# Performance work log

Measured on AMD Instinct MI355X. Metric: run time of the kernel, lower is better.

## Reference

```python
import jax, jax.numpy as jnp
import numpy as np

B, L, D = 2, 2048, 1024
DI, N, DCONV, DTR, I = 2048, 16, 4, 64, 4096  # d_inner, d_state, d_conv, dt_rank, ffn intermediate
EPS = 1e-5


def _ln(x, w, b):
    m = jnp.mean(x, axis=-1, keepdims=True)
    v = jnp.var(x, axis=-1, keepdims=True)
    return (x - m) * jax.lax.rsqrt(v + EPS) * w + b


def _mamba_dir(h, inproj_w, outproj_w, conv_w, conv_b, xproj_w, dtproj_w, dtproj_b, A_log, Dp):
    # h: (B,L,D). Standard Mamba (S6) forward for one direction.
    xz = jnp.einsum('bld,ed->ble', h, inproj_w)          # (B,L,2*DI)
    x, z = jnp.split(xz, 2, axis=-1)                     # each (B,L,DI)
    # causal depthwise conv1d, kernel size DCONV
    xp = jnp.pad(x, ((0, 0), (DCONV - 1, 0), (0, 0)))
    x = sum(xp[:, k:k + L, :] * conv_w[:, k] for k in range(DCONV)) + conv_b
    x = jax.nn.silu(x)
    x_dbl = jnp.einsum('bld,ed->ble', x, xproj_w)        # (B,L,DTR+2N)
    dt, Bm, Cm = jnp.split(x_dbl, [DTR, DTR + N], axis=-1)
    dt = jax.nn.softplus(jnp.einsum('blr,dr->bld', dt, dtproj_w) + dtproj_b)  # (B,L,DI)
    A = -jnp.exp(A_log)                                  # (DI,N)

    def step(s, inp):
        xt, dtt, bt, ct = inp                            # (B,DI),(B,DI),(B,N),(B,N)
        dA = jnp.exp(dtt[..., None] * A)                 # (B,DI,N)
        s = s * dA + (dtt * xt)[..., None] * bt[:, None, :]
        y = jnp.einsum('bdn,bn->bd', s, ct)
        return s, y

    xs = (x.transpose(1, 0, 2), dt.transpose(1, 0, 2), Bm.transpose(1, 0, 2), Cm.transpose(1, 0, 2))
    s0 = jnp.zeros((x.shape[0], DI, N), dtype=x.dtype)
    _, ys = jax.lax.scan(step, s0, xs)                   # ys: (L,B,DI)
    y = ys.transpose(1, 0, 2) + x * Dp
    y = y * jax.nn.silu(z)
    return jnp.einsum('bld,ed->ble', y, outproj_w)       # (B,L,D)


def _forward(hidden_states, residual, inproj_w, outproj_w,
             conv_w_f, conv_b_f, xproj_w_f, dtproj_w_f, dtproj_b_f, A_log_f, D_f,
             conv_w_r, conv_b_r, xproj_w_r, dtproj_w_r, dtproj_b_r, A_log_r, D_r,
             ln1_w, ln1_b, ln2_w, ln2_b, gate_w, up_w, down_w):
    # inner mamba_ssm Block: add -> LN -> mixer
    res1 = hidden_states + residual
    h = _ln(res1, ln1_w, ln1_b)
    out_f = _mamba_dir(h, inproj_w, outproj_w, conv_w_f, conv_b_f, xproj_w_f,
                       dtproj_w_f, dtproj_b_f, A_log_f, D_f)
    out_r = _mamba_dir(h[:, ::-1, :], inproj_w, outproj_w, conv_w_r, conv_b_r, xproj_w_r,
                       dtproj_w_r, dtproj_b_r, A_log_r, D_r)[:, ::-1, :]
    h = out_f + out_r                                    # bidirectional 'add'
    # outer MambaBlock: add -> LN -> MLP
    residual2 = h + res1
    h = _ln(residual2, ln2_w, ln2_b)
    gate = jax.nn.silu(jnp.einsum('bld,id->bli', h, gate_w))
    up = jnp.einsum('bld,id->bli', h, up_w)
    h = jnp.einsum('bli,di->bld', gate * up, down_w)
    return h, residual2


def setup_inputs() -> dict:
    key = jax.random.key(0)
    ks = jax.random.split(key, 24)

    def nrm(k, shape, scale=0.02):
        return jax.random.normal(k, shape, dtype=jnp.float32) * scale

    inp = {
        'hidden_states': jax.random.normal(ks[0], (B, L, D), jnp.float32),
        'residual': jax.random.normal(ks[1], (B, L, D), jnp.float32),
        'inproj_w': nrm(ks[2], (2 * DI, D)),
        'outproj_w': nrm(ks[3], (D, DI)),
    }
    for i, sfx in enumerate(('f', 'r')):
        o = 4 + i * 7
        inp[f'conv_w_{sfx}'] = nrm(ks[o], (DI, DCONV), 0.2)
        inp[f'conv_b_{sfx}'] = nrm(ks[o + 1], (DI,), 0.02)
        inp[f'xproj_w_{sfx}'] = nrm(ks[o + 2], (DTR + 2 * N, DI))
        inp[f'dtproj_w_{sfx}'] = nrm(ks[o + 3], (DI, DTR), 0.1)
        inp[f'dtproj_b_{sfx}'] = jnp.full((DI,), -4.0, jnp.float32) + nrm(ks[o + 4], (DI,), 0.1)
        inp[f'A_log_{sfx}'] = jnp.log(jnp.tile(jnp.arange(1, N + 1, dtype=jnp.float32)[None, :], (DI, 1)))
        inp[f'D_{sfx}'] = jnp.ones((DI,), jnp.float32)
    inp['ln1_w'] = jnp.ones((D,), jnp.float32)
    inp['ln1_b'] = jnp.zeros((D,), jnp.float32)
    inp['ln2_w'] = jnp.ones((D,), jnp.float32)
    inp['ln2_b'] = jnp.zeros((D,), jnp.float32)
    inp['gate_w'] = nrm(ks[18], (I, D))
    inp['up_w'] = nrm(ks[19], (I, D))
    inp['down_w'] = nrm(ks[20], (D, I))
    return inp


def reference(hidden_states, residual, inproj_w, outproj_w,
              conv_w_f, conv_b_f, xproj_w_f, dtproj_w_f, dtproj_b_f, A_log_f, D_f,
              conv_w_r, conv_b_r, xproj_w_r, dtproj_w_r, dtproj_b_r, A_log_r, D_r,
              ln1_w, ln1_b, ln2_w, ln2_b, gate_w, up_w, down_w):
    return _forward(hidden_states, residual, inproj_w, outproj_w,
                    conv_w_f, conv_b_f, xproj_w_f, dtproj_w_f, dtproj_b_f, A_log_f, D_f,
                    conv_w_r, conv_b_r, xproj_w_r, dtproj_w_r, dtproj_b_r, A_log_r, D_r,
                    ln1_w, ln1_b, ln2_w, ln2_b, gate_w, up_w, down_w)
```

## Files before the change

kernel.cpp:

```cpp
#include <hip/hip_runtime.h>
#include <hip/hip_bf16.h>

#define BB 2
#define LL 2048
#define DD 1024
#define DI_ 2048
#define NS 16
#define DTR_ 64
#define XDW 96
#define BLR 4096
#define NC 64
#define CLEN 32

typedef __attribute__((ext_vector_type(8))) short s16x8;
typedef __attribute__((ext_vector_type(4))) float f32x4;

#define L2E 1.44269504f
#define LN2 0.69314718f

__device__ __forceinline__ float bfraw2f(unsigned short u){
  union { unsigned int i; float f; } x; x.i = ((unsigned int)u) << 16; return x.f;
}
__device__ __forceinline__ unsigned short f2bfraw(float f){
  union { float f; unsigned int i; } x; x.f = f;
  unsigned int u = x.i;
  u += 0x7FFFu + ((u >> 16) & 1u);
  return (unsigned short)(u >> 16);
}
__device__ __forceinline__ float exp2_(float x){ return __builtin_amdgcn_exp2f(x); }
__device__ __forceinline__ float silu_(float a){
  float e = exp2_(-a * L2E);
  return a * __builtin_amdgcn_rcpf(1.f + e);
}
__device__ __forceinline__ float softplus_(float v){
  if (v > 20.f) return v;
  float e = exp2_(v * L2E);
  return LN2 * __builtin_amdgcn_logf(1.f + e);
}

typedef __attribute__((address_space(1))) void gas_void;
typedef __attribute__((address_space(3))) void las_void;
__device__ __forceinline__ void gl_lds16(const unsigned short* g, unsigned short* l){
  __builtin_amdgcn_global_load_lds((gas_void*)g, (las_void*)l, 16, 0, 0);
}

struct CvtArgs {
  const float* s[9];
  unsigned short* d;
  unsigned int off[10];
};
__global__ __launch_bounds__(256) void k_wcvt(CvtArgs a, unsigned int total4){
  unsigned int g = blockIdx.x*256 + threadIdx.x;
  if (g >= total4) return;
  unsigned int e = g*4;
  int sgi = 0;
  #pragma unroll
  for (int i=1;i<9;i++) if (e >= a.off[i]) sgi = i;
  const float* s = a.s[sgi];
  f32x4 v = *(const f32x4*)(s + (e - a.off[sgi]));
  unsigned long long o = 0;
  #pragma unroll
  for (int k=0;k<4;k++) o |= ((unsigned long long)f2bfraw(v[k])) << (16*k);
  *(unsigned long long*)(a.d + e) = o;
}

__global__ __launch_bounds__(256) void k_add_ln(
  const float* __restrict__ pa, const float* __restrict__ pb,
  const float* __restrict__ w, const float* __restrict__ bi,
  float* __restrict__ res_f,
  unsigned short* __restrict__ h_out)
{
  int row = blockIdx.x, tid = threadIdx.x;
  int lane = tid & 63, wave = tid >> 6;
  int c0 = tid * 4;
  size_t base = (size_t)row * DD + c0;
  float v[4];
  f32x4 av = *(const f32x4*)(pa + base);
  f32x4 bv = *(const f32x4*)(pb + base);
  #pragma unroll
  for (int k=0;k<4;k++) v[k] = av[k] + bv[k];
  float s_ = v[0]+v[1]+v[2]+v[3];
  #pragma unroll
  for (int off=32; off>0; off>>=1) s_ += __shfl_down(s_, off, 64);
  __shared__ float red1[4], red2[4];
  if (lane==0) red1[wave] = s_;
  __syncthreads();
  float mean = (red1[0]+red1[1]+red1[2]+red1[3]) * (1.f/DD);
  float ss = 0.f;
  #pragma unroll
  for (int k=0;k<4;k++){ float dv = v[k]-mean; ss += dv*dv; }
  #pragma unroll
  for (int off=32; off>0; off>>=1) ss += __shfl_down(ss, off, 64);
  if (lane==0) red2[wave] = ss;
  __syncthreads();
  float var = (red2[0]+red2[1]+red2[2]+red2[3]) * (1.f/DD);
  float rs = rsqrtf(var + 1e-5f);
  f32x4 wv = *(const f32x4*)(w + c0);
  f32x4 biv = *(const f32x4*)(bi + c0);
  unsigned long long hv = 0;
  #pragma unroll
  for (int k=0;k<4;k++){
    float hn = (v[k]-mean)*rs*wv[k] + biv[k];
    hv |= ((unsigned long long)(unsigned short)f2bfraw(hn)) << (16*k);
  }
  *(unsigned long long*)(h_out + base) = hv;
  if (res_f){ f32x4 o = {v[0],v[1],v[2],v[3]}; *(f32x4*)(res_f + base) = o; }
}

__global__ __launch_bounds__(256) void k_add_ln4(
  const float* __restrict__ pa, const float* __restrict__ pb,
  const float* __restrict__ w, const float* __restrict__ bi,
  float* __restrict__ res_f,
  unsigned short* __restrict__ h_out)
{
  int row = blockIdx.x, tid = threadIdx.x;
  int lane = tid & 63, wave = tid >> 6;
  int c0 = tid * 4;
  size_t base = (size_t)row * DD + c0;
  const size_t MN = 4194304;
  f32x4 p0 = *(const f32x4*)(pa + base);
  f32x4 p1 = *(const f32x4*)(pa + MN + base);
  f32x4 p2 = *(const f32x4*)(pa + 2*MN + base);
  f32x4 p3 = *(const f32x4*)(pa + 3*MN + base);
  f32x4 bv = *(const f32x4*)(pb + base);
  float v[4];
  #pragma unroll
  for (int k=0;k<4;k++) v[k] = ((p0[k]+p1[k]) + (p2[k]+p3[k])) + bv[k];
  float s_ = v[0]+v[1]+v[2]+v[3];
  #pragma unroll
  for (int off=32; off>0; off>>=1) s_ += __shfl_down(s_, off, 64);
  __shared__ float red1[4], red2[4];
  if (lane==0) red1[wave] = s_;
  __syncthreads();
  float mean = (red1[0]+red1[1]+red1[2]+red1[3]) * (1.f/DD);
  float ss = 0.f;
  #pragma unroll
  for (int k=0;k<4;k++){ float dv = v[k]-mean; ss += dv*dv; }
  #pragma unroll
  for (int off=32; off>0; off>>=1) ss += __shfl_down(ss, off, 64);
  if (lane==0) red2[wave] = ss;
  __syncthreads();
  float var = (red2[0]+red2[1]+red2[2]+red2[3]) * (1.f/DD);
  float rs = rsqrtf(var + 1e-5f);
  f32x4 wv = *(const f32x4*)(w + c0);
  f32x4 biv = *(const f32x4*)(bi + c0);
  unsigned long long hv = 0;
  #pragma unroll
  for (int k=0;k<4;k++){
    float hn = (v[k]-mean)*rs*wv[k] + biv[k];
    hv |= ((unsigned long long)(unsigned short)f2bfraw(hn)) << (16*k);
  }
  *(unsigned long long*)(h_out + base) = hv;
  if (res_f){ f32x4 o = {v[0],v[1],v[2],v[3]}; *(f32x4*)(res_f + base) = o; }
}

__global__ __launch_bounds__(256) void k_red4(
  const float* __restrict__ p, float* __restrict__ o)
{
  size_t e = ((size_t)blockIdx.x*256 + threadIdx.x)*4;
  const size_t MN = 4194304;
  f32x4 a = *(const f32x4*)(p + e);
  f32x4 b = *(const f32x4*)(p + MN + e);
  f32x4 c = *(const f32x4*)(p + 2*MN + e);
  f32x4 d = *(const f32x4*)(p + 3*MN + e);
  f32x4 r;
  #pragma unroll
  for (int k=0;k<4;k++) r[k] = (a[k]+b[k]) + (c[k]+d[k]);
  *(f32x4*)(o + e) = r;
}

template<int EPI>
__global__ __launch_bounds__(256) void k_gemm_lds(
  const unsigned short* __restrict__ A0, const unsigned short* __restrict__ A1,
  const unsigned short* __restrict__ W0, const unsigned short* __restrict__ W1,
  float* __restrict__ Cf0, float* __restrict__ Cf1,
  unsigned short* __restrict__ Cb0, unsigned short* __restrict__ Cb1,
  const float* __restrict__ bias0, const float* __restrict__ bias1,
  int M, int N, int K, int lda)
{
  __shared__ unsigned short S[17408];
  const unsigned short* A = blockIdx.z ? A1 : A0;
  const unsigned short* W = blockIdx.z ? W1 : W0;
  float* Cf = blockIdx.z ? Cf1 : Cf0;
  unsigned short* Cb = blockIdx.z ? Cb1 : Cb0;
  const float* bias = blockIdx.z ? bias1 : bias0;

  int tid = threadIdx.x;
  int wave = tid >> 6, lane = tid & 63;
  int l16 = lane & 15, quad = lane >> 4;
  int wm = (wave >> 1) * 64, wn = (wave & 1) * 64;
  int m0 = blockIdx.y * 128, n0 = blockIdx.x * 128;

  int colsw = (((lane & 7) ^ (lane >> 3)) * 8);
  const unsigned short* ag[4];
  const unsigned short* wg[4];
  unsigned short* al[4];
  unsigned short* bl[4];
  #pragma unroll
  for (int c = 0; c < 4; c++){
    int ca = wave*4 + c;
    int ra = m0 + ca*8 + (lane>>3); if (ra >= M) ra = M-1;
    int rb = n0 + ca*8 + (lane>>3); if (rb >= N) rb = N-1;
    ag[c] = A + (size_t)ra*lda + colsw;
    wg[c] = W + (size_t)rb*K + colsw;
    al[c] = S + ca*512;
    bl[c] = S + 8192 + ca*512;
  }

  int swz = (l16 & 7) * 8;
  f32x4 acc[4][4] = {};

  for (int k0 = 0; k0 < K; k0 += 64){
    #pragma unroll
    for (int c = 0; c < 4; c++){
      gl_lds16(ag[c] + k0, al[c]);
      gl_lds16(wg[c] + k0, bl[c]);
    }
    __syncthreads();
    #pragma unroll
    for (int s = 0; s < 2; s++){
      int koff = (s*32 + quad*8) ^ swz;
      s16x8 af[4], bw[4];
      #pragma unroll
      for (int i = 0; i < 4; i++)
        af[i] = *(const s16x8*)(S + (wm + i*16 + l16)*64 + koff);
      #pragma unroll
      for (int j = 0; j < 4; j++)
        bw[j] = *(const s16x8*)(S + 8192 + (wn + j*16 + l16)*64 + koff);
      #pragma unroll
      for (int i = 0; i < 4; i++)
        #pragma unroll
        for (int j = 0; j < 4; j++)
          acc[i][j] = __builtin_amdgcn_mfma_f32_16x16x32_bf16(af[i], bw[j], acc[i][j], 0, 0, 0);
    }
    __syncthreads();
  }

  if (Cb){
    #pragma unroll
    for (int j=0;j<4;j++){
      int colL = wn + j*16 + l16;
      float bval = (EPI==1) ? bias[n0 + colL] : 0.f;
      #pragma unroll
      for (int i=0;i<4;i++){
        #pragma unroll
        for (int r=0;r<4;r++){
          int rowL = wm + i*16 + quad*4 + r;
          float v = acc[i][j][r];
          if (EPI==1) v = softplus_(v + bval);
          S[rowL*136 + colL] = f2bfraw(v);
        }
      }
    }
    __syncthreads();
    #pragma unroll
    for (int p=0;p<8;p++){
      int e = p*2048 + tid*8;
      int rowL = e >> 7, colL = e & 127;
      s16x8 val = *(const s16x8*)(S + rowL*136 + colL);
      *(s16x8*)(Cb + (size_t)(m0 + rowL)*N + n0 + colL) = val;
    }
  } else {
    #pragma unroll
    for (int j=0;j<4;j++){
      int col = n0 + wn + j*16 + l16;
      if (col >= N) continue;
      float bval = (EPI==1) ? bias[col] : 0.f;
      #pragma unroll
      for (int i=0;i<4;i++){
        #pragma unroll
        for (int r=0;r<4;r++){
          int rowi = m0 + wm + i*16 + quad*4 + r;
          float v = acc[i][j][r];
          if (EPI==1) v = softplus_(v + bval);
          Cf[(size_t)rowi*N + col] = v;
        }
      }
    }
  }
}

__global__ __launch_bounds__(256) void k_gemm_sk2(
  const unsigned short* __restrict__ A, const unsigned short* __restrict__ W,
  float* __restrict__ P,
  int M, int N, int K, int lda, int kwin)
{
  __shared__ unsigned short S[16384];
  int tid = threadIdx.x;
  int wave = tid >> 6, lane = tid & 63;
  int l16 = lane & 15, quad = lane >> 4;
  int wm = (wave >> 1) * 64, wn = (wave & 1) * 64;

  int bid = blockIdx.x;
  int xcd = bid & 7;
  int idx = bid >> 3;
  int nt  = idx & 7;
  int ks  = (idx >> 3) & 3;
  int mg  = idx >> 5;
  int m0 = (xcd*4 + mg) * 128;
  int n0 = nt * 128;
  int kbase = ks * kwin;
  float* Cf = P + (size_t)ks * ((size_t)M * N);

  int colsw = (((lane & 7) ^ (lane >> 3)) * 8);
  const unsigned short* ag[4];
  const unsigned short* wg[4];
  unsigned short* al[4];
  unsigned short* bl[4];
  #pragma unroll
  for (int c = 0; c < 4; c++){
    int ca = wave*4 + c;
    int ra = m0 + ca*8 + (lane>>3);
    int rb = n0 + ca*8 + (lane>>3);
    ag[c] = A + (size_t)ra*lda + kbase + colsw;
    wg[c] = W + (size_t)rb*K + kbase + colsw;
    al[c] = S + ca*512;
    bl[c] = S + 8192 + ca*512;
  }

  int swz = (l16 & 7) * 8;
  f32x4 acc[4][4] = {};

  for (int k0 = 0; k0 < kwin; k0 += 64){
    #pragma unroll
    for (int c = 0; c < 4; c++){
      gl_lds16(ag[c] + k0, al[c]);
      gl_lds16(wg[c] + k0, bl[c]);
    }
    __syncthreads();
    #pragma unroll
    for (int s = 0; s < 2; s++){
      int koff = (s*32 + quad*8) ^ swz;
      s16x8 af[4], bw[4];
      #pragma unroll
      for (int i = 0; i < 4; i++)
        af[i] = *(const s16x8*)(S + (wm + i*16 + l16)*64 + koff);
      #pragma unroll
      for (int j = 0; j < 4; j++)
        bw[j] = *(const s16x8*)(S + 8192 + (wn + j*16 + l16)*64 + koff);
      #pragma unroll
      for (int i = 0; i < 4; i++)
        #pragma unroll
        for (int j = 0; j < 4; j++)
          acc[i][j] = __builtin_amdgcn_mfma_f32_16x16x32_bf16(af[i], bw[j], acc[i][j], 0, 0, 0);
    }
    __syncthreads();
  }

  #pragma unroll
  for (int j=0;j<4;j++){
    int col = n0 + wn + j*16 + l16;
    #pragma unroll
    for (int i=0;i<4;i++){
      #pragma unroll
      for (int r=0;r<4;r++){
        int rowi = m0 + wm + i*16 + quad*4 + r;
        Cf[(size_t)rowi*N + col] = acc[i][j][r];
      }
    }
  }
}

__global__ __launch_bounds__(512) void k_gemm_gateup(
  const unsigned short* __restrict__ A, const unsigned short* __restrict__ Wg,
  const unsigned short* __restrict__ Wu, unsigned short* __restrict__ Cb,
  int M, int N, int K, int lda)
{
  __shared__ unsigned short S[24576];
  int tid = threadIdx.x;
  int wave = tid >> 6, lane = tid & 63;
  int l16 = lane & 15, quad = lane >> 4;
  int w4 = wave & 3;
  int isUp = wave >> 2;
  int wm = (w4 >> 1) * 64, wn = (w4 & 1) * 64;
  int m0 = blockIdx.y * 128, n0 = blockIdx.x * 128;

  int colsw = (((lane & 7) ^ (lane >> 3)) * 8);
  const unsigned short* ag[2];
  const unsigned short* gg[2];
  const unsigned short* ug[2];
  unsigned short* al[2];
  unsigned short* glp[2];
  unsigned short* ulp[2];
  #pragma unroll
  for (int c = 0; c < 2; c++){
    int ca = wave*2 + c;
    int ra = m0 + ca*8 + (lane>>3);
    int rb = n0 + ca*8 + (lane>>3);
    ag[c] = A + (size_t)ra*lda + colsw;
    gg[c] = Wg + (size_t)rb*K + colsw;
    ug[c] = Wu + (size_t)rb*K + colsw;
    al[c]  = S + ca*512;
    glp[c] = S + 8192 + ca*512;
    ulp[c] = S + 16384 + ca*512;
  }

  int swz = (l16 & 7) * 8;
  int bbase = isUp ? 16384 : 8192;
  f32x4 acc[4][4] = {};

  for (int k0 = 0; k0 < K; k0 += 64){
    #pragma unroll
    for (int c = 0; c < 2; c++){
      gl_lds16(ag[c] + k0, al[c]);
      gl_lds16(gg[c] + k0, glp[c]);
      gl_lds16(ug[c] + k0, ulp[c]);
    }
    __syncthreads();
    #pragma unroll
    for (int s = 0; s < 2; s++){
      int koff = (s*32 + quad*8) ^ swz;
      s16x8 af[4], bw[4];
      #pragma unroll
      for (int i = 0; i < 4; i++)
        af[i] = *(const s16x8*)(S + (wm + i*16 + l16)*64 + koff);
      #pragma unroll
      for (int j = 0; j < 4; j++)
        bw[j] = *(const s16x8*)(S + bbase + (wn + j*16 + l16)*64 + koff);
      #pragma unroll
      for (int i = 0; i < 4; i++)
        #pragma unroll
        for (int j = 0; j < 4; j++)
          acc[i][j] = __builtin_amdgcn_mfma_f32_16x16x32_bf16(af[i], bw[j], acc[i][j], 0, 0, 0);
    }
    __syncthreads();
  }

  if (isUp){
    #pragma unroll
    for (int j=0;j<4;j++){
      int colL = wn + j*16 + l16;
      #pragma unroll
      for (int i=0;i<4;i++){
        #pragma unroll
        for (int r=0;r<4;r++){
          int rowL = wm + i*16 + quad*4 + r;
          S[rowL*136 + colL] = f2bfraw(acc[i][j][r]);
        }
      }
    }
  }
  __syncthreads();
  if (!isUp){
    #pragma unroll
    for (int j=0;j<4;j++){
      int colL = wn + j*16 + l16;
      #pragma unroll
      for (int i=0;i<4;i++){
        #pragma unroll
        for (int r=0;r<4;r++){
          int rowL = wm + i*16 + quad*4 + r;
          int idx = rowL*136 + colL;
          float u = bfraw2f(S[idx]);
          S[idx] = f2bfraw(silu_(acc[i][j][r]) * u);
        }
      }
    }
  }
  __syncthreads();
  #pragma unroll
  for (int p=0;p<4;p++){
    int e = p*4096 + tid*8;
    int rowL = e >> 7, colL = e & 127;
    s16x8 val = *(const s16x8*)(S + rowL*136 + colL);
    *(s16x8*)(Cb + (size_t)(m0 + rowL)*N + n0 + colL) = val;
  }
}

__global__ __launch_bounds__(256) void k_gemm_splitk(
  const unsigned short* __restrict__ A0, const unsigned short* __restrict__ A1,
  const unsigned short* __restrict__ W0, const unsigned short* __restrict__ W1,
  float* __restrict__ C0, float* __restrict__ C1,
  int M, int N, int K, int lda, int kwin)
{
  __shared__ unsigned short S[16384];
  const unsigned short* A = blockIdx.z ? A1 : A0;
  const unsigned short* W = blockIdx.z ? W1 : W0;
  float* C = blockIdx.z ? C1 : C0;

  int tid = threadIdx.x;
  int wave = tid >> 6, lane = tid & 63;
  int l16 = lane & 15, quad = lane >> 4;
  int wm = (wave >> 1) * 64, wn = (wave & 1) * 64;
  int m0 = blockIdx.y * 128;
  int kbase = blockIdx.x * kwin;

  int colsw = (((lane & 7) ^ (lane >> 3)) * 8);
  const unsigned short* ag[4];
  const unsigned short* wg[4];
  unsigned short* al[4];
  unsigned short* bl[4];
  #pragma unroll
  for (int c = 0; c < 4; c++){
    int ca = wave*4 + c;
    int ra = m0 + ca*8 + (lane>>3);
    int rb = ca*8 + (lane>>3); if (rb >= N) rb = N-1;
    ag[c] = A + (size_t)ra*lda + kbase + colsw;
    wg[c] = W + (size_t)rb*K + kbase + colsw;
    al[c] = S + ca*512;
    bl[c] = S + 8192 + ca*512;
  }

  int swz = (l16 & 7) * 8;
  f32x4 acc[4][4] = {};

  for (int k0 = 0; k0 < kwin; k0 += 64){
    #pragma unroll
    for (int c = 0; c < 4; c++){
      gl_lds16(ag[c] + k0, al[c]);
      gl_lds16(wg[c] + k0, bl[c]);
    }
    __syncthreads();
    #pragma unroll
    for (int s = 0; s < 2; s++){
      int koff = (s*32 + quad*8) ^ swz;
      s16x8 af[4], bw[4];
      #pragma unroll
      for (int i = 0; i < 4; i++)
        af[i] = *(const s16x8*)(S + (wm + i*16 + l16)*64 + koff);
      #pragma unroll
      for (int j = 0; j < 4; j++)
        bw[j] = *(const s16x8*)(S + 8192 + (wn + j*16 + l16)*64 + koff);
      #pragma unroll
      for (int i = 0; i < 4; i++)
        #pragma unroll
        for (int j = 0; j < 4; j++)
          acc[i][j] = __builtin_amdgcn_mfma_f32_16x16x32_bf16(af[i], bw[j], acc[i][j], 0, 0, 0);
    }
    __syncthreads();
  }

  #pragma unroll
  for (int j=0;j<4;j++){
    int col = wn + j*16 + l16;
    if (col >= N) continue;
    #pragma unroll
    for (int i=0;i<4;i++){
      #pragma unroll
      for (int r=0;r<4;r++){
        int rowi = m0 + wm + i*16 + quad*4 + r;
        atomicAdd(&C[(size_t)rowi*N + col], acc[i][j][r]);
      }
    }
  }
}

__global__ __launch_bounds__(256) void k_xdcvt(
  const float* __restrict__ xd, unsigned short* __restrict__ xdb)
{
  unsigned int e = (blockIdx.x*256 + threadIdx.x)*4;
  f32x4 v = *(const f32x4*)(xd + e);
  unsigned long long o = 0;
  #pragma unroll
  for (int k=0;k<4;k++) o |= ((unsigned long long)f2bfraw(v[k])) << (16*k);
  *(unsigned long long*)(xdb + e) = o;
}

__global__ __launch_bounds__(256) void k_conv(
  const unsigned short* __restrict__ xz,
  const float* __restrict__ cw0, const float* __restrict__ cb0,
  const float* __restrict__ cw1, const float* __restrict__ cb1,
  unsigned short* __restrict__ xc0, unsigned short* __restrict__ xc1)
{
  int row = blockIdx.x;
  int dir = blockIdx.y;
  int b = row >> 11, t = row & (LL-1);
  int d0 = threadIdx.x * 8;
  const float* cw = dir ? cw1 : cw0;
  const float* cb = dir ? cb1 : cb0;
  unsigned short* xc = dir ? xc1 : xc0;

  float acc[8];
  #pragma unroll
  for (int ii=0;ii<8;ii++) acc[ii] = cb[d0+ii];
  float wv[8][4];
  #pragma unroll
  for (int ii=0;ii<8;ii++)
    #pragma unroll
    for (int k=0;k<4;k++) wv[ii][k] = cw[(d0+ii)*4 + k];

  #pragma unroll
  for (int k=0;k<4;k++){
    int j = t - 3 + k;
    if (j < 0) continue;
    int in_row = dir ? (LL-1-j) : j;
    union { s16x8 v; unsigned short e[8]; } xu;
    xu.v = *(const s16x8*)(xz + ((size_t)(b*LL + in_row))*4096 + d0);
    #pragma unroll
    for (int ii=0;ii<8;ii++) acc[ii] += wv[ii][k] * bfraw2f(xu.e[ii]);
  }
  union { s16x8 v; unsigned short e[8]; } ou;
  #pragma unroll
  for (int ii=0;ii<8;ii++) ou.e[ii] = f2bfraw(silu_(acc[ii]));
  *(s16x8*)(xc + (size_t)row*DI_ + d0) = ou.v;
}

__global__ __launch_bounds__(256) void k_scan1(
  const unsigned short* __restrict__ xc0, const unsigned short* __restrict__ xc1,
  const unsigned short* __restrict__ dt0, const unsigned short* __restrict__ dt1,
  const float* __restrict__ xd0, const float* __restrict__ xd1,
  const float* __restrict__ al0, const float* __restrict__ al1,
  float* __restrict__ cP, float* __restrict__ cS)
{
  int dir = blockIdx.z >> 1, b = blockIdx.z & 1;
  int c = blockIdx.y;
  int d = blockIdx.x*256 + threadIdx.x;
  const unsigned short* xc = dir ? xc1 : xc0;
  const unsigned short* dt = dir ? dt1 : dt0;
  const float* xd = dir ? xd1 : xd0;
  const float* al = dir ? al1 : al0;

  __shared__ float bc[CLEN*32];
  size_t rb = ((size_t)(b*LL + c*CLEN))*XDW + DTR_;
  for (int idx = threadIdx.x; idx < CLEN*32; idx += 256){
    int tl = idx >> 5, col = idx & 31;
    bc[idx] = xd[rb + (size_t)tl*XDW + col];
  }
  __syncthreads();

  float a2[NS], s[NS];
  bool okb = true;
  #pragma unroll
  for (int n=0;n<NS;n++){
    float e = exp2_(al[d*NS+n]*L2E);
    a2[n] = -e * L2E;
    s[n] = 0.f;
    if (n > 0) okb = okb && (fabsf(a2[n] - (float)(n+1)*a2[0]) <= 1e-4f*fabsf(a2[n]) + 1e-6f);
  }
  bool ok = (__all(okb) != 0);
  float a20 = a2[0];
  float sdt = 0.f;
  size_t rowb = (size_t)(b*LL + c*CLEN)*DI_ + d;
  if (ok){
    for (int tl=0; tl<CLEN; tl++){
      float dtv = bfraw2f(dt[rowb]);
      float xv  = bfraw2f(xc[rowb]);
      rowb += DI_;
      float dtx = dtv*xv;
      sdt += dtv;
      float e1 = exp2_(dtv*a20);
      float da = e1;
      const float* bcp = &bc[tl*32];
      #pragma unroll
      for (int n=0;n<NS;n++){
        s[n] = s[n]*da + dtx*bcp[n];
        da *= e1;
      }
    }
  } else {
    for (int tl=0; tl<CLEN; tl++){
      float dtv = bfraw2f(dt[rowb]);
      float xv  = bfraw2f(xc[rowb]);
      rowb += DI_;
      float dtx = dtv*xv;
      sdt += dtv;
      const float* bcp = &bc[tl*32];
      #pragma unroll
      for (int n=0;n<NS;n++){
        float da = exp2_(dtv*a2[n]);
        s[n] = s[n]*da + dtx*bcp[n];
      }
    }
  }
  float P[NS];
  if (ok){
    float pe = exp2_(sdt*a20);
    float pc = pe;
    #pragma unroll
    for (int n=0;n<NS;n++){ P[n] = pc; pc *= pe; }
  } else {
    #pragma unroll
    for (int n=0;n<NS;n++) P[n] = exp2_(sdt*a2[n]);
  }
  size_t ob = ((size_t)(blockIdx.z*NC + c)*DI_ + d)*NS;
  #pragma unroll
  for (int q=0;q<4;q++){
    f32x4 tp = {P[q*4],P[q*4+1],P[q*4+2],P[q*4+3]};
    f32x4 ts = {s[q*4],s[q*4+1],s[q*4+2],s[q*4+3]};
    *(f32x4*)(cP+ob+q*4) = tp;
    *(f32x4*)(cS+ob+q*4) = ts;
  }
}

__global__ __launch_bounds__(256) void k_scan2(
  float* __restrict__ cP, const float* __restrict__ cS)
{
  int gid = blockIdx.x*256 + threadIdx.x;
  int n = gid & 15;
  int d = (gid >> 4) & 2047;
  int db = gid >> 15;
  const size_t cstride = (size_t)DI_*NS;
  size_t base = (size_t)db*NC*cstride + (size_t)d*NS + n;
  float cur = 0.f;
  for (int c=1;c<NC;c++){
    size_t prev = base + (size_t)(c-1)*cstride;
    cur = cS[prev] + cP[prev]*cur;
    cP[prev] = cur;
  }
}

__global__ __launch_bounds__(256) void k_scan3(
  const unsigned short* __restrict__ xc0, const unsigned short* __restrict__ xc1,
  const unsigned short* __restrict__ dt0, const unsigned short* __restrict__ dt1,
  const float* __restrict__ xd0, const float* __restrict__ xd1,
  const float* __restrict__ al0, const float* __restrict__ al1,
  const float* __restrict__ Dp0, const float* __restrict__ Dp1,
  const float* __restrict__ cP,
  unsigned short* __restrict__ y_f, unsigned short* __restrict__ y_r)
{
  int dir = blockIdx.z >> 1, b = blockIdx.z & 1;
  int c = blockIdx.y;
  int d = blockIdx.x*256 + threadIdx.x;
  const unsigned short* xc = dir ? xc1 : xc0;
  const unsigned short* dt = dir ? dt1 : dt0;
  const float* xd = dir ? xd1 : xd0;
  const float* al = dir ? al1 : al0;
  const float* Dp = dir ? Dp1 : Dp0;
  unsigned short* y = dir ? y_r : y_f;

  __shared__ float bc[CLEN*32];
  size_t rb = ((size_t)(b*LL + c*CLEN))*XDW + DTR_;
  for (int idx = threadIdx.x; idx < CLEN*32; idx += 256){
    int tl = idx >> 5, col = idx & 31;
    bc[idx] = xd[rb + (size_t)tl*XDW + col];
  }
  __syncthreads();

  float a2[NS], s[NS];
  const size_t cstride = (size_t)DI_*NS;
  size_t sb = (size_t)blockIdx.z*NC*cstride + (size_t)(c-1)*cstride + (size_t)d*NS;
  bool okb = true;
  #pragma unroll
  for (int n=0;n<NS;n++){
    float e = exp2_(al[d*NS+n]*L2E);
    a2[n] = -e * L2E;
    s[n] = (c == 0) ? 0.f : cP[sb + n];
    if (n > 0) okb = okb && (fabsf(a2[n] - (float)(n+1)*a2[0]) <= 1e-4f*fabsf(a2[n]) + 1e-6f);
  }
  bool ok = (__all(okb) != 0);
  float a20 = a2[0];
  float Dd = Dp[d];
  size_t rowb = (size_t)(b*LL + c*CLEN)*DI_ + d;
  if (ok){
    for (int tl=0; tl<CLEN; tl++){
      float dtv = bfraw2f(dt[rowb]);
      float xv  = bfraw2f(xc[rowb]);
      float dtx = dtv*xv;
      const float* bcp = &bc[tl*32];
      float e1 = exp2_(dtv*a20);
      float da = e1;
      float yv = 0.f;
      #pragma unroll
      for (int n=0;n<NS;n++){
        s[n] = s[n]*da + dtx*bcp[n];
        yv += s[n]*bcp[16+n];
        da *= e1;
      }
      y[rowb] = f2bfraw(yv + xv*Dd);
      rowb += DI_;
    }
  } else {
    for (int tl=0; tl<CLEN; tl++){
      float dtv = bfraw2f(dt[rowb]);
      float xv  = bfraw2f(xc[rowb]);
      float dtx = dtv*xv;
      const float* bcp = &bc[tl*32];
      float yv = 0.f;
      #pragma unroll
      for (int n=0;n<NS;n++){
        float da = exp2_(dtv*a2[n]);
        s[n] = s[n]*da + dtx*bcp[n];
        yv += s[n]*bcp[16+n];
      }
      y[rowb] = f2bfraw(yv + xv*Dd);
      rowb += DI_;
    }
  }
}

__global__ __launch_bounds__(256) void k_combine(
  const unsigned short* __restrict__ y_f, const unsigned short* __restrict__ y_r,
  const unsigned short* __restrict__ xz, unsigned short* __restrict__ o)
{
  size_t i = ((size_t)blockIdx.x*256 + threadIdx.x)*4;
  size_t row = i >> 11;
  int d = (int)(i & 2047);
  int b = (int)(row >> 11), t = (int)(row & (LL-1));
  size_t rrow = (size_t)(b*LL + (LL-1-t));
  unsigned long long yfv = *(const unsigned long long*)(y_f + i);
  unsigned long long yrv = *(const unsigned long long*)(y_r + rrow*DI_ + d);
  unsigned long long zv = *(const unsigned long long*)(xz + row*4096 + 2048 + d);
  unsigned long long ov = 0;
  #pragma unroll
  for (int k=0;k<4;k++){
    float tot = bfraw2f((unsigned short)(yfv >> (16*k))) + bfraw2f((unsigned short)(yrv >> (16*k)));
    float z = bfraw2f((unsigned short)(zv >> (16*k)));
    ov |= ((unsigned long long)(unsigned short)f2bfraw(tot*silu_(z))) << (16*k);
  }
  *(unsigned long long*)(o + i) = ov;
}

extern "C" void kernel_launch(void* const* d_in, const int* in_sizes, int n_in,
                              void* d_out, int out_size, void* d_ws, size_t ws_size,
                              hipStream_t stream)
{
  typedef const float* cfp;
  cfp hs = (cfp)d_in[0], res = (cfp)d_in[1], inproj = (cfp)d_in[2], outproj = (cfp)d_in[3];
  cfp conv_w_f=(cfp)d_in[4],  cfp_conv_b_f=(cfp)d_in[5],  xproj_f=(cfp)d_in[6],  dtw_f=(cfp)d_in[7],
      dtb_f=(cfp)d_in[8],     alog_f=(cfp)d_in[9],    Dp_f=(cfp)d_in[10];
  cfp conv_w_r=(cfp)d_in[11], conv_b_r=(cfp)d_in[12], xproj_r=(cfp)d_in[13], dtw_r=(cfp)d_in[14],
      dtb_r=(cfp)d_in[15],    alog_r=(cfp)d_in[16],   Dp_r=(cfp)d_in[17];
  cfp ln1w=(cfp)d_in[18], ln1b=(cfp)d_in[19], ln2w=(cfp)d_in[20], ln2b=(cfp)d_in[21];
  cfp gw=(cfp)d_in[22], uw=(cfp)d_in[23], dwn=(cfp)d_in[24];
  cfp conv_b_f = cfp_conv_b_f;

  char* ws = (char*)d_ws;
  float*          res1    = (float*)(ws + 0);
  unsigned short* xz      = (unsigned short*)(ws + 16777216);
  unsigned short* xcf     = (unsigned short*)(ws + 50331648);
  unsigned short* xcr     = (unsigned short*)(ws + 67108864);
  float*          xdf     = (float*)(ws + 83886080);
  float*          xdr     = (float*)(ws + 85458944);
  unsigned short* xdbf    = (unsigned short*)(ws + 87031808);
  unsigned short* xdbr    = (unsigned short*)(ws + 87818240);
  unsigned short* h_bf    = (unsigned short*)(ws + 88604672);
  unsigned short* dtf     = (unsigned short*)(ws + 88604672);
  unsigned short* ysum_bf = (unsigned short*)(ws + 88604672);
  unsigned short* dtr     = (unsigned short*)(ws + 105381888);
  float*          cP      = (float*)(ws + 122159104);
  float*          cS      = (float*)(ws + 155713536);
  unsigned short* ysum_f  = (unsigned short*)(ws + 155713536);
  unsigned short* ysum_r  = (unsigned short*)(ws + 189267968);
  unsigned short* wb      = (unsigned short*)(ws + 206045184);
  unsigned short* act_bf  = (unsigned short*)(ws + 16777216);
  float*          P_out   = (float*)(ws + 122159104);
  float*          P_dn    = (float*)(ws + 50331648);
  float* out0f = (float*)d_out;
  float* out1f = out0f + 4194304;

  unsigned short* inprojb = wb + 0;
  unsigned short* outprojb= wb + 4194304;
  unsigned short* xprojbf = wb + 6291456;
  unsigned short* xprojbr = wb + 6488064;
  unsigned short* dtwbf   = wb + 6684672;
  unsigned short* dtwbr   = wb + 6815744;
  unsigned short* gwb     = wb + 6946816;
  unsigned short* uwb     = wb + 11141120;
  unsigned short* dwnb    = wb + 15335424;

  CvtArgs ca;
  ca.s[0]=inproj; ca.s[1]=outproj; ca.s[2]=xproj_f; ca.s[3]=xproj_r; ca.s[4]=dtw_f;
  ca.s[5]=dtw_r;  ca.s[6]=gw;      ca.s[7]=uw;      ca.s[8]=dwn;
  ca.d = wb;
  unsigned int offs[10] = {0u,4194304u,6291456u,6488064u,6684672u,6815744u,
                           6946816u,11141120u,15335424u,19529728u};
  for (int i=0;i<10;i++) ca.off[i]=offs[i];
  k_wcvt<<<19072, 256, 0, stream>>>(ca, 4882432u);
  hipMemsetAsync(ws + 83886080, 0, 3145728, stream);

  k_add_ln<<<BLR, 256, 0, stream>>>(hs, res, ln1w, ln1b, res1, h_bf);
  k_gemm_lds<0><<<dim3(32,32,1),256,0,stream>>>(h_bf,h_bf, inprojb,inprojb,
      nullptr,nullptr, xz,xz, nullptr,nullptr, BLR, 4096, 1024, 1024);
  k_conv<<<dim3(BLR,2),256,0,stream>>>(xz, conv_w_f, conv_b_f, conv_w_r, conv_b_r, xcf, xcr);
  k_gemm_splitk<<<dim3(8,32,2),256,0,stream>>>(xcf,xcr, xprojbf,xprojbr,
      xdf,xdr, BLR, XDW, 2048, 2048, 256);
  k_xdcvt<<<768,256,0,stream>>>(xdf, xdbf);
  k_gemm_lds<1><<<dim3(16,32,2),256,0,stream>>>(xdbf,xdbr, dtwbf,dtwbr,
      nullptr,nullptr, dtf,dtr, dtb_f,dtb_r, BLR, DI_, DTR_, XDW);
  k_scan1<<<dim3(8,NC,4),256,0,stream>>>(xcf,xcr, dtf,dtr, xdf,xdr, alog_f,alog_r, cP, cS);
  k_scan2<<<512,256,0,stream>>>(cP, cS);
  k_scan3<<<dim3(8,NC,4),256,0,stream>>>(xcf,xcr, dtf,dtr, xdf,xdr, alog_f,alog_r,
      Dp_f,Dp_r, cP, ysum_f, ysum_r);
  k_combine<<<8192,256,0,stream>>>(ysum_f, ysum_r, xz, ysum_bf);
  k_gemm_sk2<<<1024,256,0,stream>>>(ysum_bf, outprojb, P_out,
      BLR, DD, 2048, 2048, 512);
  k_add_ln4<<<BLR, 256, 0, stream>>>(P_out, res1, ln2w, ln2b, out1f, h_bf);
  k_gemm_gateup<<<dim3(32,32),512,0,stream>>>(h_bf, gwb, uwb, act_bf,
      BLR, 4096, 1024, 1024);
  k_gemm_sk2<<<1024,256,0,stream>>>(act_bf, dwnb, P_dn,
      BLR, DD, 4096, 4096, 1024);
  k_red4<<<4096,256,0,stream>>>(P_dn, out0f);
}
```

Before: 674.2 us.

## Cut split-K slices, replace x_proj atomics with partial buffers, tile conv over time

The out_proj and down_proj split-K GEMMs go from 4 to 2 K-slices, which halves the partial-sum traffic read back by the LayerNorm and reduce kernels but leaves fewer blocks. The x_proj split-K GEMM now writes its 8 slices to separate partial buffers instead of using atomicAdd. A conversion kernel sums those slices and writes both fp32 and bf16, which also removes the memset. The causal conv kernel now handles 8 timesteps per thread with a sliding register window, so each input row is read about once instead of four times.

```diff
diff --git a/kernel.cpp b/kernel.cpp
--- a/kernel.cpp
+++ b/kernel.cpp
@@ -107,7 +107,7 @@
   if (res_f){ f32x4 o = {v[0],v[1],v[2],v[3]}; *(f32x4*)(res_f + base) = o; }
 }
 
-__global__ __launch_bounds__(256) void k_add_ln4(
+__global__ __launch_bounds__(256) void k_add_ln2(
   const float* __restrict__ pa, const float* __restrict__ pb,
   const float* __restrict__ w, const float* __restrict__ bi,
   float* __restrict__ res_f,
@@ -120,12 +120,10 @@
   const size_t MN = 4194304;
   f32x4 p0 = *(const f32x4*)(pa + base);
   f32x4 p1 = *(const f32x4*)(pa + MN + base);
-  f32x4 p2 = *(const f32x4*)(pa + 2*MN + base);
-  f32x4 p3 = *(const f32x4*)(pa + 3*MN + base);
   f32x4 bv = *(const f32x4*)(pb + base);
   float v[4];
   #pragma unroll
-  for (int k=0;k<4;k++) v[k] = ((p0[k]+p1[k]) + (p2[k]+p3[k])) + bv[k];
+  for (int k=0;k<4;k++) v[k] = (p0[k]+p1[k]) + bv[k];
   float s_ = v[0]+v[1]+v[2]+v[3];
   #pragma unroll
   for (int off=32; off>0; off>>=1) s_ += __shfl_down(s_, off, 64);
@@ -154,18 +152,16 @@
   if (res_f){ f32x4 o = {v[0],v[1],v[2],v[3]}; *(f32x4*)(res_f + base) = o; }
 }
 
-__global__ __launch_bounds__(256) void k_red4(
+__global__ __launch_bounds__(256) void k_red2(
   const float* __restrict__ p, float* __restrict__ o)
 {
   size_t e = ((size_t)blockIdx.x*256 + threadIdx.x)*4;
   const size_t MN = 4194304;
   f32x4 a = *(const f32x4*)(p + e);
   f32x4 b = *(const f32x4*)(p + MN + e);
-  f32x4 c = *(const f32x4*)(p + 2*MN + e);
-  f32x4 d = *(const f32x4*)(p + 3*MN + e);
   f32x4 r;
   #pragma unroll
-  for (int k=0;k<4;k++) r[k] = (a[k]+b[k]) + (c[k]+d[k]);
+  for (int k=0;k<4;k++) r[k] = a[k]+b[k];
   *(f32x4*)(o + e) = r;
 }
 
@@ -283,7 +279,7 @@
 __global__ __launch_bounds__(256) void k_gemm_sk2(
   const unsigned short* __restrict__ A, const unsigned short* __restrict__ W,
   float* __restrict__ P,
-  int M, int N, int K, int lda, int kwin)
+  int M, int N, int K, int lda, int kwin, int nsl)
 {
   __shared__ unsigned short S[16384];
   int tid = threadIdx.x;
@@ -295,8 +291,8 @@
   int xcd = bid & 7;
   int idx = bid >> 3;
   int nt  = idx & 7;
-  int ks  = (idx >> 3) & 3;
-  int mg  = idx >> 5;
+  int ks  = (idx >> 3) & ((1<<nsl)-1);
+  int mg  = idx >> (3+nsl);
   int m0 = (xcd*4 + mg) * 128;
   int n0 = nt * 128;
   int kbase = ks * kwin;
@@ -470,13 +466,14 @@
 __global__ __launch_bounds__(256) void k_gemm_splitk(
   const unsigned short* __restrict__ A0, const unsigned short* __restrict__ A1,
   const unsigned short* __restrict__ W0, const unsigned short* __restrict__ W1,
-  float* __restrict__ C0, float* __restrict__ C1,
+  float* __restrict__ P,
   int M, int N, int K, int lda, int kwin)
 {
   __shared__ unsigned short S[16384];
   const unsigned short* A = blockIdx.z ? A1 : A0;
   const unsigned short* W = blockIdx.z ? W1 : W0;
-  float* C = blockIdx.z ? C1 : C0;
+  size_t MN = (size_t)M * N;
+  float* C = P + (size_t)blockIdx.x * (2*MN) + (size_t)blockIdx.z * MN;
 
   int tid = threadIdx.x;
   int wave = tid >> 6, lane = tid & 63;
@@ -539,60 +536,106 @@
       #pragma unroll
       for (int r=0;r<4;r++){
         int rowi = m0 + wm + i*16 + quad*4 + r;
-        atomicAdd(&C[(size_t)rowi*N + col], acc[i][j][r]);
+        C[(size_t)rowi*N + col] = acc[i][j][r];
       }
     }
   }
 }
 
-__global__ __launch_bounds__(256) void k_xdcvt(
-  const float* __restrict__ xd, unsigned short* __restrict__ xdb)
+__global__ __launch_bounds__(256) void k_xdcvt8(
+  const float* __restrict__ p, float* __restrict__ xd, unsigned short* __restrict__ xdb)
 {
   unsigned int e = (blockIdx.x*256 + threadIdx.x)*4;
-  f32x4 v = *(const f32x4*)(xd + e);
+  f32x4 s = {0.f,0.f,0.f,0.f};
+  #pragma unroll
+  for (int q=0;q<8;q++){
+    f32x4 v = *(const f32x4*)(p + (size_t)q*786432u + e);
+    #pragma unroll
+    for (int k=0;k<4;k++) s[k] += v[k];
+  }
+  *(f32x4*)(xd + e) = s;
   unsigned long long o = 0;
   #pragma unroll
-  for (int k=0;k<4;k++) o |= ((unsigned long long)f2bfraw(v[k])) << (16*k);
+  for (int k=0;k<4;k++) o |= ((unsigned long long)f2bfraw(s[k])) << (16*k);
   *(unsigned long long*)(xdb + e) = o;
 }
 
-__global__ __launch_bounds__(256) void k_conv(
+__global__ __launch_bounds__(256) void k_conv2(
   const unsigned short* __restrict__ xz,
   const float* __restrict__ cw0, const float* __restrict__ cb0,
   const float* __restrict__ cw1, const float* __restrict__ cb1,
   unsigned short* __restrict__ xc0, unsigned short* __restrict__ xc1)
 {
-  int row = blockIdx.x;
+  int g = blockIdx.x;
   int dir = blockIdx.y;
-  int b = row >> 11, t = row & (LL-1);
+  int b = g >> 8, t0 = (g & 255) * 8;
   int d0 = threadIdx.x * 8;
   const float* cw = dir ? cw1 : cw0;
   const float* cb = dir ? cb1 : cb0;
   unsigned short* xc = dir ? xc1 : xc0;
 
-  float acc[8];
-  #pragma unroll
-  for (int ii=0;ii<8;ii++) acc[ii] = cb[d0+ii];
-  float wv[8][4];
-  #pragma unroll
-  for (int ii=0;ii<8;ii++)
+  float bias[8], wv[8][4];
+  #pragma unroll
+  for (int ii=0;ii<8;ii++){
+    bias[ii] = cb[d0+ii];
     #pragma unroll
     for (int k=0;k<4;k++) wv[ii][k] = cw[(d0+ii)*4 + k];
-
-  #pragma unroll
-  for (int k=0;k<4;k++){
-    int j = t - 3 + k;
-    if (j < 0) continue;
-    int in_row = dir ? (LL-1-j) : j;
-    union { s16x8 v; unsigned short e[8]; } xu;
-    xu.v = *(const s16x8*)(xz + ((size_t)(b*LL + in_row))*4096 + d0);
-    #pragma unroll
-    for (int ii=0;ii<8;ii++) acc[ii] += wv[ii][k] * bfraw2f(xu.e[ii]);
-  }
-  union { s16x8 v; unsigned short e[8]; } ou;
-  #pragma unroll
-  for (int ii=0;ii<8;ii++) ou.e[ii] = f2bfraw(silu_(acc[ii]));
-  *(s16x8*)(xc + (size_t)row*DI_ + d0) = ou.v;
+  }
+
+  float win0[8], win1[8], win2[8];
+  #pragma unroll
+  for (int ii=0;ii<8;ii++){ win0[ii]=0.f; win1[ii]=0.f; win2[ii]=0.f; }
+  {
+    int j = t0 - 3;
+    if (j >= 0){
+      int ir = dir ? (LL-1-j) : j;
+      union { s16x8 v; unsigned short e[8]; } xu;
+      xu.v = *(const s16x8*)(xz + ((size_t)(b*LL + ir))*4096 + d0);
+      #pragma unroll
+      for (int ii=0;ii<8;ii++) win0[ii] = bfraw2f(xu.e[ii]);
+    }
+  }
+  {
+    int j = t0 - 2;
+    if (j >= 0){
+      int ir = dir ? (LL-1-j) : j;
+      union { s16x8 v; unsigned short e[8]; } xu;
+      xu.v = *(const s16x8*)(xz + ((size_t)(b*LL + ir))*4096 + d0);
+      #pragma unroll
+      for (int ii=0;ii<8;ii++) win1[ii] = bfraw2f(xu.e[ii]);
+    }
+  }
+  {
+    int j = t0 - 1;
+    if (j >= 0){
+      int ir = dir ? (LL-1-j) : j;
+      union { s16x8 v; unsigned short e[8]; } xu;
+      xu.v = *(const s16x8*)(xz + ((size_t)(b*LL + ir))*4096 + d0);
+      #pragma unroll
+      for (int ii=0;ii<8;ii++) win2[ii] = bfraw2f(xu.e[ii]);
+    }
+  }
+
+  #pragma unroll
+  for (int tt=0; tt<8; tt++){
+    int j = t0 + tt;
+    int ir = dir ? (LL-1-j) : j;
+    union { s16x8 v; unsigned short e[8]; } cu;
+    cu.v = *(const s16x8*)(xz + ((size_t)(b*LL + ir))*4096 + d0);
+    float cur[8];
+    #pragma unroll
+    for (int ii=0;ii<8;ii++) cur[ii] = bfraw2f(cu.e[ii]);
+    union { s16x8 v; unsigned short e[8]; } ou;
+    #pragma unroll
+    for (int ii=0;ii<8;ii++){
+      float a = bias[ii] + wv[ii][0]*win0[ii] + wv[ii][1]*win1[ii]
+                        + wv[ii][2]*win2[ii] + wv[ii][3]*cur[ii];
+      ou.e[ii] = f2bfraw(silu_(a));
+    }
+    *(s16x8*)(xc + ((size_t)(b*LL + j))*DI_ + d0) = ou.v;
+    #pragma unroll
+    for (int ii=0;ii<8;ii++){ win0[ii]=win1[ii]; win1[ii]=win2[ii]; win2[ii]=cur[ii]; }
+  }
 }
 
 __global__ __launch_bounds__(256) void k_scan1(
@@ -833,6 +876,7 @@
   unsigned short* ysum_r  = (unsigned short*)(ws + 189267968);
   unsigned short* wb      = (unsigned short*)(ws + 206045184);
   unsigned short* act_bf  = (unsigned short*)(ws + 16777216);
+  float*          P_xd    = (float*)(ws + 122159104);
   float*          P_out   = (float*)(ws + 122159104);
   float*          P_dn    = (float*)(ws + 50331648);
   float* out0f = (float*)d_out;
@@ -856,15 +900,14 @@
                            6946816u,11141120u,15335424u,19529728u};
   for (int i=0;i<10;i++) ca.off[i]=offs[i];
   k_wcvt<<<19072, 256, 0, stream>>>(ca, 4882432u);
-  hipMemsetAsync(ws + 83886080, 0, 3145728, stream);
 
   k_add_ln<<<BLR, 256, 0, stream>>>(hs, res, ln1w, ln1b, res1, h_bf);
   k_gemm_lds<0><<<dim3(32,32,1),256,0,stream>>>(h_bf,h_bf, inprojb,inprojb,
       nullptr,nullptr, xz,xz, nullptr,nullptr, BLR, 4096, 1024, 1024);
-  k_conv<<<dim3(BLR,2),256,0,stream>>>(xz, conv_w_f, conv_b_f, conv_w_r, conv_b_r, xcf, xcr);
+  k_conv2<<<dim3(512,2),256,0,stream>>>(xz, conv_w_f, conv_b_f, conv_w_r, conv_b_r, xcf, xcr);
   k_gemm_splitk<<<dim3(8,32,2),256,0,stream>>>(xcf,xcr, xprojbf,xprojbr,
-      xdf,xdr, BLR, XDW, 2048, 2048, 256);
-  k_xdcvt<<<768,256,0,stream>>>(xdf, xdbf);
+      P_xd, BLR, XDW, 2048, 2048, 256);
+  k_xdcvt8<<<768,256,0,stream>>>(P_xd, xdf, xdbf);
   k_gemm_lds<1><<<dim3(16,32,2),256,0,stream>>>(xdbf,xdbr, dtwbf,dtwbr,
       nullptr,nullptr, dtf,dtr, dtb_f,dtb_r, BLR, DI_, DTR_, XDW);
   k_scan1<<<dim3(8,NC,4),256,0,stream>>>(xcf,xcr, dtf,dtr, xdf,xdr, alog_f,alog_r, cP, cS);
@@ -872,12 +915,12 @@
   k_scan3<<<dim3(8,NC,4),256,0,stream>>>(xcf,xcr, dtf,dtr, xdf,xdr, alog_f,alog_r,
       Dp_f,Dp_r, cP, ysum_f, ysum_r);
   k_combine<<<8192,256,0,stream>>>(ysum_f, ysum_r, xz, ysum_bf);
-  k_gemm_sk2<<<1024,256,0,stream>>>(ysum_bf, outprojb, P_out,
-      BLR, DD, 2048, 2048, 512);
-  k_add_ln4<<<BLR, 256, 0, stream>>>(P_out, res1, ln2w, ln2b, out1f, h_bf);
+  k_gemm_sk2<<<512,256,0,stream>>>(ysum_bf, outprojb, P_out,
+      BLR, DD, 2048, 2048, 1024, 1);
+  k_add_ln2<<<BLR, 256, 0, stream>>>(P_out, res1, ln2w, ln2b, out1f, h_bf);
   k_gemm_gateup<<<dim3(32,32),512,0,stream>>>(h_bf, gwb, uwb, act_bf,
       BLR, 4096, 1024, 1024);
-  k_gemm_sk2<<<1024,256,0,stream>>>(act_bf, dwnb, P_dn,
-      BLR, DD, 4096, 4096, 1024);
-  k_red4<<<4096,256,0,stream>>>(P_dn, out0f);
-}
+  k_gemm_sk2<<<512,256,0,stream>>>(act_bf, dwnb, P_dn,
+      BLR, DD, 4096, 4096, 2048, 1);
+  k_red2<<<4096,256,0,stream>>>(P_dn, out0f);
+}
```

After: 574.1 us. 14.8% less time.
